# Optimization experiments

Measured on AMD Instinct MI355X. Metric: run time of the kernel, lower is better.

The kernel has to match this reference:

```python
import jax, jax.numpy as jnp
import numpy as np

T = 4096
MOL = 2048
DESC = 6
NSOL = 5
H = 2048
D_BLOCK = MOL + DESC            # 2054
FUSE = D_BLOCK * (1 + NSOL)     # 12324
D_IN = FUSE + 1                 # 12325
BOUNDARY_RF = 0.5
CLAMP_LO, CLAMP_HI = 1e-4, 1.0 - 1e-4


def setup_inputs() -> dict:
    key = jax.random.key(0)
    ks = jax.random.split(key, 32)
    s = 0.02  # weight init scale for numerical stability
    d = {
        "mol_vec": jax.random.normal(ks[0], (MOL,), jnp.float32),
        "solvent_seq": jax.random.uniform(ks[1], (T, NSOL), jnp.float32),
        "desc_seq": jax.random.normal(ks[2], (T, DESC), jnp.float32),
        "rf_true": jax.random.uniform(ks[3], (T,), jnp.float32),
        "solvent_vecs": jax.random.normal(ks[4], (NSOL, MOL), jnp.float32),
    }
    wshapes = [
        ("Wf0", (H, D_IN)), ("Wf1", (H, H)), ("Wf2", (H, H)), ("Wof", (1, H)),
        ("Wb0", (H, D_IN)), ("Wb1", (H, H)), ("Wb2", (H, H)), ("Wob", (1, H)),
    ]
    for i, (name, shp) in enumerate(wshapes):
        d[name] = jax.random.normal(ks[5 + i], shp, jnp.float32) * s
    for name, shp in [("bf0", (H,)), ("bf1", (H,)), ("bf2", (H,)), ("bof", (1,)),
                      ("bb0", (H,)), ("bb1", (H,)), ("bb2", (H,)), ("bob", (1,))]:
        d[name] = jnp.zeros(shp, jnp.float32)
    return d


def _step_features(mol_vec, solvent_seq, desc_seq, solvent_vecs):
    # mol_vec [MOL]; solvent_seq [T,NSOL]; desc_seq [T,DESC]; solvent_vecs [NSOL,MOL]
    mol_cat = jnp.concatenate(
        [jnp.broadcast_to(mol_vec, (T, MOL)), desc_seq], axis=-1)  # [T, D_BLOCK]
    scaled = solvent_seq[:, :, None] * solvent_vecs[None, :, :]      # [T,NSOL,MOL]
    sol_block = jnp.concatenate(
        [scaled, jnp.broadcast_to(desc_seq[:, None, :], (T, NSOL, DESC))], axis=-1)
    sol_flat = sol_block.reshape(T, NSOL * D_BLOCK)
    return jnp.concatenate([mol_cat, sol_flat], axis=-1)             # [T, FUSE]


def _trunk(x, W0, b0, W1, b1, W2, b2):
    # 3 Linear+GELU blocks (dropout is identity in eval)
    h = jax.nn.gelu(x @ W0.T + b0, approximate=False)
    h = jax.nn.gelu(h @ W1.T + b1, approximate=False)
    h = jax.nn.gelu(h @ W2.T + b2, approximate=False)
    return h


def reference(mol_vec, solvent_seq, desc_seq, rf_true, solvent_vecs,
              Wf0, bf0, Wf1, bf1, Wf2, bf2, Wof, bof,
              Wb0, bb0, Wb1, bb1, Wb2, bb2, Wob, bob):
    x = _step_features(mol_vec, solvent_seq, desc_seq, solvent_vecs)  # [T, FUSE]
    rf = jax.lax.stop_gradient(rf_true)  # teacher signal is detached
    b = jnp.asarray([BOUNDARY_RF], dtype=x.dtype)
    prev = jnp.concatenate([b, rf[:-1]])  # fwd branch sees rf_true[t-1]
    nxt = jnp.concatenate([rf[1:], b])    # bwd branch sees rf_true[t+1]

    inp_f = jnp.concatenate([x, prev[:, None]], axis=-1)  # [T, D_IN]
    inp_b = jnp.concatenate([x, nxt[:, None]], axis=-1)

    hf = _trunk(inp_f, Wf0, bf0, Wf1, bf1, Wf2, bf2)
    hb = _trunk(inp_b, Wb0, bb0, Wb1, bb1, Wb2, bb2)
    rf_fwd = (hf @ Wof.T + bof).squeeze(-1)  # [T]
    rf_bwd = (hb @ Wob.T + bob).squeeze(-1)
    rf_fwd = jnp.clip(rf_fwd, CLAMP_LO, CLAMP_HI)
    rf_bwd = jnp.clip(rf_bwd, CLAMP_LO, CLAMP_HI)
    return rf_fwd, rf_bwd
```

## Files before the change

kernel.cpp:

```cpp
#include <hip/hip_runtime.h>
#include <hip/hip_fp16.h>
#include <math.h>

#define T_DIM 4096
#define MOL_N 2048
#define DESC_N 6
#define NSOL_N 5
#define H_DIM 2048
#define DBLK 2054
#define D_IN_N 12325
#define GK 2048

typedef _Float16 f16x8 __attribute__((ext_vector_type(8)));
typedef float f32x4 __attribute__((ext_vector_type(4)));

__device__ __forceinline__ float gelu_f(float x) {
    float v = x * (1.5957691f + 0.0713548f * x * x);
    float e = __expf(-v);
    return x / (1.0f + e);
}

__global__ __launch_bounds__(256) void fold2_kernel(
    const float* __restrict__ W0f, const float* __restrict__ W0b,
    const float* __restrict__ b0f, const float* __restrict__ b0b,
    const float* __restrict__ mol, const float* __restrict__ sv,
    float* __restrict__ fold_f, float* __restrict__ fold_b)
{
    __shared__ float wrow[13312];
    __shared__ float red[4][6];
    const int tid = threadIdx.x;
    const int wave = tid >> 6, lane = tid & 63;
    const size_t matbytes = (size_t)2048 * D_IN_N * 4;
    char* wrc = (char*)wrow;

    for (int rr = 0; rr < 4; ++rr) {
        const int r = blockIdx.x + rr * 1024;
        const int z = r >> 11, h = r & 2047;
        const float* __restrict__ W0 = z ? W0b : W0f;
        const float* __restrict__ b0 = z ? b0b : b0f;
        float* __restrict__ fold = z ? fold_b : fold_f;
        const size_t rowdw = (size_t)h * D_IN_N;
        const size_t A0 = rowdw & ~(size_t)3;
        const int p = (int)(rowdw & 3);
        const size_t A0byte = A0 * 4;
        const char* __restrict__ W0c = (const char*)W0;

        #pragma unroll
        for (int j = 0; j < 13; ++j) {
            const size_t off = (size_t)j * 4096 + (size_t)wave * 1024 + (size_t)lane * 16;
            size_t g = A0byte + off;
            if (g + 16 > matbytes) g = A0byte;
            __builtin_amdgcn_global_load_lds(
                (const __attribute__((address_space(1))) void*)(W0c + g),
                (__attribute__((address_space(3))) void*)(wrc + off), 16, 0, 0);
        }
        asm volatile("s_waitcnt vmcnt(0)" ::: "memory");
        __syncthreads();

        float acc[6] = {0.f, 0.f, 0.f, 0.f, 0.f, 0.f};
        #pragma unroll
        for (int s = 0; s < 6; ++s) {
            const int cb = (s == 0) ? 0 : DBLK * s;
            const float* __restrict__ xp = (s == 0) ? mol : (sv + (size_t)(s - 1) * MOL_N);
            #pragma unroll
            for (int q = 0; q < 8; ++q) {
                const int col = tid + q * 256;
                acc[s] += wrow[p + cb + col] * xp[col];
            }
        }
        #pragma unroll
        for (int i = 0; i < 6; ++i) {
            float v = acc[i];
            #pragma unroll
            for (int off = 32; off >= 1; off >>= 1)
                v += __shfl_xor(v, off, 64);
            acc[i] = v;
        }
        if (lane == 0) {
            #pragma unroll
            for (int i = 0; i < 6; ++i) red[wave][i] = acc[i];
        }
        __syncthreads();
        if (tid < 6) {
            float s = red[0][tid] + red[1][tid] + red[2][tid] + red[3][tid];
            if (tid == 0) fold[h] = s + b0[h];
            else fold[(size_t)tid * H_DIM + h] = s;
        }
        if (tid >= 64 && tid < 70) {
            const int j = tid - 64;
            float w = wrow[p + MOL_N + j];
            #pragma unroll
            for (int s = 1; s <= 5; ++s) w += wrow[p + DBLK * s + MOL_N + j];
            fold[(size_t)(6 + j) * H_DIM + h] = w;
        }
        if (tid == 70) fold[(size_t)12 * H_DIM + h] = wrow[p + D_IN_N - 1];
        __syncthreads();
    }
}

__global__ __launch_bounds__(256) void conv_kernel(
    const float* __restrict__ W1f, const float* __restrict__ W2f,
    const float* __restrict__ W1b, const float* __restrict__ W2b,
    _Float16* __restrict__ Wc)
{
    const int b = blockIdx.x;
    const int z = b >> 10;
    const float* __restrict__ src = (z == 0) ? W1f : (z == 1) ? W2f : (z == 2) ? W1b : W2b;
    _Float16* __restrict__ dst = Wc + (size_t)z * H_DIM * H_DIM;
    const int base4 = (b & 1023) * 1024;
    struct h4 { _Float16 a, b, c, d; };
    #pragma unroll
    for (int k = 0; k < 4; ++k) {
        const int i4 = base4 + k * 256 + threadIdx.x;
        float4 v = ((const float4*)src)[i4];
        h4 o;
        o.a = (_Float16)v.x; o.b = (_Float16)v.y; o.c = (_Float16)v.z; o.d = (_Float16)v.w;
        ((h4*)dst)[i4] = o;
    }
}

__global__ __launch_bounds__(256) void h0_kernel(
    const float* __restrict__ fold_f, const float* __restrict__ fold_b,
    const float* __restrict__ desc, const float* __restrict__ sol,
    const float* __restrict__ rf,
    _Float16* __restrict__ h0f, _Float16* __restrict__ h0b)
{
    const int z = blockIdx.z;
    const float* __restrict__ fold = z ? fold_b : fold_f;
    _Float16* __restrict__ h0 = z ? h0b : h0f;
    const int hb = blockIdx.x * 1024 + threadIdx.x * 4;
    const int tbase = blockIdx.y * 64;

    float c0a[4], wpa[4], ua[NSOL_N][4], wda[DESC_N][4];
    {
        float4 v = *(const float4*)&fold[hb];
        c0a[0] = v.x; c0a[1] = v.y; c0a[2] = v.z; c0a[3] = v.w;
        v = *(const float4*)&fold[(size_t)12 * H_DIM + hb];
        wpa[0] = v.x; wpa[1] = v.y; wpa[2] = v.z; wpa[3] = v.w;
        #pragma unroll
        for (int s = 0; s < NSOL_N; ++s) {
            v = *(const float4*)&fold[(size_t)(1 + s) * H_DIM + hb];
            ua[s][0] = v.x; ua[s][1] = v.y; ua[s][2] = v.z; ua[s][3] = v.w;
        }
        #pragma unroll
        for (int j = 0; j < DESC_N; ++j) {
            v = *(const float4*)&fold[(size_t)(6 + j) * H_DIM + hb];
            wda[j][0] = v.x; wda[j][1] = v.y; wda[j][2] = v.z; wda[j][3] = v.w;
        }
    }

    struct h4s { _Float16 a, b, c, d; };
    for (int i = 0; i < 64; ++i) {
        const int t = tbase + i;
        float pv;
        if (z == 0) pv = (t == 0) ? 0.5f : rf[t - 1];
        else        pv = (t == T_DIM - 1) ? 0.5f : rf[t + 1];
        float sl[NSOL_N], dc[DESC_N];
        #pragma unroll
        for (int s = 0; s < NSOL_N; ++s) sl[s] = sol[t * NSOL_N + s];
        #pragma unroll
        for (int j = 0; j < DESC_N; ++j) dc[j] = desc[t * DESC_N + j];
        float o[4];
        #pragma unroll
        for (int e = 0; e < 4; ++e) {
            float pre = c0a[e] + wpa[e] * pv;
            #pragma unroll
            for (int s = 0; s < NSOL_N; ++s) pre += ua[s][e] * sl[s];
            #pragma unroll
            for (int j = 0; j < DESC_N; ++j) pre += wda[j][e] * dc[j];
            o[e] = gelu_f(pre);
        }
        h4s ov;
        ov.a = (_Float16)o[0]; ov.b = (_Float16)o[1];
        ov.c = (_Float16)o[2]; ov.d = (_Float16)o[3];
        *(h4s*)&h0[(size_t)t * H_DIM + hb] = ov;
    }
}

__device__ __forceinline__ void gemm_core256(
    const _Float16* __restrict__ A, const _Float16* __restrict__ W,
    const int m0, const int n0, char* sc, f32x4 (&acc)[8][4])
{
    const int tid = threadIdx.x;
    const int wave = tid >> 6;
    const int lane = tid & 63;
    const int t15 = lane & 15;
    const int quad = lane >> 4;
    const int wr = wave >> 2;
    const int wc = wave & 3;
    const int poff = (quad ^ ((t15 >> 1) & 3)) * 16;
    const int aoff0 = (wr * 128 + t15) * 64 + poff;
    const int boff0 = 16384 + (wc * 64 + t15) * 64 + poff;

    const _Float16* gsrc[4];
    #pragma unroll
    for (int ld = 0; ld < 4; ++ld) {
        const int j = (ld & 1) * 512 + tid;
        const int r = j >> 2;
        const int c = (j & 3) ^ ((r >> 1) & 3);
        gsrc[ld] = ((ld < 2) ? (A + (size_t)(m0 + r) * GK)
                             : (W + (size_t)(n0 + r) * GK)) + c * 8;
    }

    #pragma unroll
    for (int mi = 0; mi < 8; ++mi)
        #pragma unroll
        for (int ni = 0; ni < 4; ++ni)
            acc[mi][ni] = (f32x4){0.f, 0.f, 0.f, 0.f};

#define STAGE_T(kt, b) do { \
    char* _db = sc + (b) * 32768; \
    const int _ko = (kt) * 32; \
    __builtin_amdgcn_global_load_lds((const __attribute__((address_space(1))) void*)(gsrc[0] + _ko), (__attribute__((address_space(3))) void*)(_db + wave * 1024), 16, 0, 0); \
    __builtin_amdgcn_global_load_lds((const __attribute__((address_space(1))) void*)(gsrc[1] + _ko), (__attribute__((address_space(3))) void*)(_db + 8192 + wave * 1024), 16, 0, 0); \
    __builtin_amdgcn_global_load_lds((const __attribute__((address_space(1))) void*)(gsrc[2] + _ko), (__attribute__((address_space(3))) void*)(_db + 16384 + wave * 1024), 16, 0, 0); \
    __builtin_amdgcn_global_load_lds((const __attribute__((address_space(1))) void*)(gsrc[3] + _ko), (__attribute__((address_space(3))) void*)(_db + 24576 + wave * 1024), 16, 0, 0); \
} while (0)

#define COMPUTE_T(b) do { \
    const char* _db = sc + (b) * 32768; \
    f16x8 aF[8], bF[4]; \
    _Pragma("unroll") \
    for (int mi = 0; mi < 8; ++mi) aF[mi] = *(const f16x8*)(_db + aoff0 + mi * 1024); \
    _Pragma("unroll") \
    for (int ni = 0; ni < 4; ++ni) bF[ni] = *(const f16x8*)(_db + boff0 + ni * 1024); \
    __builtin_amdgcn_s_setprio(1); \
    _Pragma("unroll") \
    for (int mi = 0; mi < 8; ++mi) { \
        _Pragma("unroll") \
        for (int ni = 0; ni < 4; ++ni) \
            acc[mi][ni] = __builtin_amdgcn_mfma_f32_16x16x32_f16(aF[mi], bF[ni], acc[mi][ni], 0, 0, 0); \
    } \
    __builtin_amdgcn_s_setprio(0); \
    asm volatile("s_waitcnt lgkmcnt(0)" ::: "memory"); \
} while (0)

    STAGE_T(0, 0); STAGE_T(1, 1); STAGE_T(2, 2);

    #pragma unroll 1
    for (int k4 = 0; k4 < 60; k4 += 4) {
        asm volatile("s_waitcnt vmcnt(8)" ::: "memory");
        __builtin_amdgcn_s_barrier();
        STAGE_T(k4 + 3, 3); COMPUTE_T(0);
        asm volatile("s_waitcnt vmcnt(8)" ::: "memory");
        __builtin_amdgcn_s_barrier();
        STAGE_T(k4 + 4, 0); COMPUTE_T(1);
        asm volatile("s_waitcnt vmcnt(8)" ::: "memory");
        __builtin_amdgcn_s_barrier();
        STAGE_T(k4 + 5, 1); COMPUTE_T(2);
        asm volatile("s_waitcnt vmcnt(8)" ::: "memory");
        __builtin_amdgcn_s_barrier();
        STAGE_T(k4 + 6, 2); COMPUTE_T(3);
    }
    asm volatile("s_waitcnt vmcnt(8)" ::: "memory");
    __builtin_amdgcn_s_barrier();
    STAGE_T(63, 3); COMPUTE_T(0);
    asm volatile("s_waitcnt vmcnt(8)" ::: "memory");
    __builtin_amdgcn_s_barrier();
    COMPUTE_T(1);
    asm volatile("s_waitcnt vmcnt(4)" ::: "memory");
    __builtin_amdgcn_s_barrier();
    COMPUTE_T(2);
    asm volatile("s_waitcnt vmcnt(0)" ::: "memory");
    __builtin_amdgcn_s_barrier();
    COMPUTE_T(3);

#undef STAGE_T
#undef COMPUTE_T
}

__global__ __launch_bounds__(512, 2) void gemm1_kernel(
    const _Float16* __restrict__ Af, const _Float16* __restrict__ Ab,
    const _Float16* __restrict__ Wfp, const _Float16* __restrict__ Wbp,
    const float* __restrict__ bfp, const float* __restrict__ bbp,
    _Float16* __restrict__ Cf, _Float16* __restrict__ Cb)
{
    __shared__ _Float16 smem[65536];
    char* sc = (char*)smem;
    const int bid = blockIdx.x;
    const int xcd = bid & 7;
    const int slot = bid >> 3;
    const int z = xcd & 1;
    const int q = xcd >> 1;
    const int m0 = (q * 4 + (slot & 3)) * 256;
    const int n0 = (slot >> 2) * 256;

    const _Float16* __restrict__ A = z ? Ab : Af;
    const _Float16* __restrict__ W = z ? Wbp : Wfp;
    const float* __restrict__ bias = z ? bbp : bfp;
    _Float16* __restrict__ C = z ? Cb : Cf;

    f32x4 acc[8][4];
    gemm_core256(A, W, m0, n0, sc, acc);

    const int tid = threadIdx.x;
    const int wave = tid >> 6, lane = tid & 63;
    const int colC = lane & 15, quad = lane >> 4;
    const int wr = wave >> 2, wc = wave & 3;
    #pragma unroll
    for (int ni = 0; ni < 4; ++ni) {
        const int n = n0 + wc * 64 + ni * 16 + colC;
        const float bv = bias[n];
        #pragma unroll
        for (int mi = 0; mi < 8; ++mi) {
            const int mb = m0 + wr * 128 + mi * 16 + quad * 4;
            #pragma unroll
            for (int r = 0; r < 4; ++r)
                C[(size_t)(mb + r) * H_DIM + n] = (_Float16)gelu_f(acc[mi][ni][r] + bv);
        }
    }
}

__global__ __launch_bounds__(512, 2) void gemm_out_kernel(
    const _Float16* __restrict__ Af, const _Float16* __restrict__ Ab,
    const _Float16* __restrict__ Wfp, const _Float16* __restrict__ Wbp,
    const float* __restrict__ bfp, const float* __restrict__ bbp,
    const float* __restrict__ Wof, const float* __restrict__ Wob,
    float* __restrict__ partial)
{
    __shared__ _Float16 smem[65536];
    char* sc = (char*)smem;
    const int bid = blockIdx.x;
    const int xcd = bid & 7;
    const int slot = bid >> 3;
    const int z = xcd & 1;
    const int q = xcd >> 1;
    const int m0 = (q * 4 + (slot & 3)) * 256;
    const int n0 = (slot >> 2) * 256;

    const _Float16* __restrict__ A = z ? Ab : Af;
    const _Float16* __restrict__ W = z ? Wbp : Wfp;
    const float* __restrict__ bias = z ? bbp : bfp;
    const float* __restrict__ Wo = z ? Wob : Wof;

    f32x4 acc[8][4];
    gemm_core256(A, W, m0, n0, sc, acc);

    const int tid = threadIdx.x;
    const int wave = tid >> 6, lane = tid & 63;
    const int colC = lane & 15, quad = lane >> 4;
    const int wr = wave >> 2, wc = wave & 3;

    float bv[4], wo[4];
    #pragma unroll
    for (int ni = 0; ni < 4; ++ni) {
        const int n = n0 + wc * 64 + ni * 16 + colC;
        bv[ni] = bias[n];
        wo[ni] = Wo[n];
    }

    __syncthreads();
    float* red = (float*)sc;
    #pragma unroll
    for (int mi = 0; mi < 8; ++mi) {
        #pragma unroll
        for (int r = 0; r < 4; ++r) {
            float s = 0.f;
            #pragma unroll
            for (int ni = 0; ni < 4; ++ni)
                s += gelu_f(acc[mi][ni][r] + bv[ni]) * wo[ni];
            s += __shfl_xor(s, 1, 64);
            s += __shfl_xor(s, 2, 64);
            s += __shfl_xor(s, 4, 64);
            s += __shfl_xor(s, 8, 64);
            if (colC == 0)
                red[wc * 256 + wr * 128 + mi * 16 + quad * 4 + r] = s;
        }
    }
    __syncthreads();
    if (tid < 256) {
        float v = red[tid] + red[256 + tid] + red[512 + tid] + red[768 + tid];
        const int n_tile = slot >> 2;
        partial[((size_t)z * 8 + n_tile) * T_DIM + m0 + tid] = v;
    }
}

__global__ __launch_bounds__(256) void finalize_kernel(
    const float* __restrict__ partial,
    const float* __restrict__ bof, const float* __restrict__ bob,
    float* __restrict__ out)
{
    const int idx = blockIdx.x * 256 + threadIdx.x;
    const int z = idx >> 12;
    const int row = idx & 4095;
    float v = z ? bob[0] : bof[0];
    #pragma unroll
    for (int nt = 0; nt < 8; ++nt)
        v += partial[((size_t)z * 8 + nt) * T_DIM + row];
    v = fminf(fmaxf(v, 1e-4f), 1.0f - 1e-4f);
    out[idx] = v;
}

extern "C" void kernel_launch(void* const* d_in, const int* in_sizes, int n_in,
                              void* d_out, int out_size, void* d_ws, size_t ws_size,
                              hipStream_t stream)
{
    (void)in_sizes; (void)n_in; (void)out_size; (void)ws_size;
    const float* mol = (const float*)d_in[0];
    const float* sol = (const float*)d_in[1];
    const float* desc = (const float*)d_in[2];
    const float* rf  = (const float*)d_in[3];
    const float* sv  = (const float*)d_in[4];
    const float* Wf0 = (const float*)d_in[5];
    const float* Wf1 = (const float*)d_in[6];
    const float* Wf2 = (const float*)d_in[7];
    const float* Wof = (const float*)d_in[8];
    const float* Wb0 = (const float*)d_in[9];
    const float* Wb1 = (const float*)d_in[10];
    const float* Wb2 = (const float*)d_in[11];
    const float* Wob = (const float*)d_in[12];
    const float* bf0 = (const float*)d_in[13];
    const float* bf1 = (const float*)d_in[14];
    const float* bf2 = (const float*)d_in[15];
    const float* bof = (const float*)d_in[16];
    const float* bb0 = (const float*)d_in[17];
    const float* bb1 = (const float*)d_in[18];
    const float* bb2 = (const float*)d_in[19];
    const float* bob = (const float*)d_in[20];
    float* out = (float*)d_out;

    char* ws = (char*)d_ws;
    float* fold_f = (float*)(ws + 0);
    float* fold_b = (float*)(ws + 131072);
    _Float16* Wc = (_Float16*)(ws + 262144);
    const size_t WSZ = (size_t)H_DIM * H_DIM;
    _Float16* W1f_c = Wc;
    _Float16* W2f_c = Wc + WSZ;
    _Float16* W1b_c = Wc + 2 * WSZ;
    _Float16* W2b_c = Wc + 3 * WSZ;
    const size_t HSZ = (size_t)T_DIM * H_DIM;
    _Float16* h0f = (_Float16*)(ws + 33816576);
    _Float16* h0b = h0f + HSZ;
    _Float16* h1f = (_Float16*)(ws + 33816576 + 2 * 16777216);
    _Float16* h1b = h1f + HSZ;
    float* partial = (float*)(ws + 33816576);

    fold2_kernel<<<dim3(1024), 256, 0, stream>>>(Wf0, Wb0, bf0, bb0, mol, sv, fold_f, fold_b);
    conv_kernel<<<dim3(4096), 256, 0, stream>>>(Wf1, Wf2, Wb1, Wb2, Wc);
    h0_kernel<<<dim3(2, 64, 2), 256, 0, stream>>>(fold_f, fold_b, desc, sol, rf, h0f, h0b);
    gemm1_kernel<<<dim3(256), 512, 0, stream>>>(h0f, h0b, W1f_c, W1b_c, bf1, bb1, h1f, h1b);
    gemm_out_kernel<<<dim3(256), 512, 0, stream>>>(h1f, h1b, W2f_c, W2b_c, bf2, bb2, Wof, Wob, partial);
    finalize_kernel<<<dim3(32), 256, 0, stream>>>(partial, bof, bob, out);
}
```

Before: 469.8 us.

## Split fold kernel across row-segments grid and remap GEMM tiles per XCD

The first-layer weight fold kernel, which looped over 4 rows per block with an LDS staging buffer, is replaced by a 4096x6 grid where each block reduces one 2048-column segment of one row straight from global memory. This raises parallelism and removes the 52KB LDS footprint, which should help the bandwidth-bound read of the two large first-layer weight matrices, at the cost of more blocks and unaligned global reads. The GEMM block-to-tile mapping also changes so that each XCD covers all M tiles for two N tiles rather than four M tiles for all N tiles, which changes L2 reuse of the weight versus activation panels.

Result: slower. 487.3 us (+3.7%).

```diff
diff --git a/kernel.cpp b/kernel.cpp
--- a/kernel.cpp
+++ b/kernel.cpp
@@ -20,81 +20,51 @@
     return x / (1.0f + e);
 }
 
-__global__ __launch_bounds__(256) void fold2_kernel(
+__global__ __launch_bounds__(256) void fold3_kernel(
     const float* __restrict__ W0f, const float* __restrict__ W0b,
     const float* __restrict__ b0f, const float* __restrict__ b0b,
     const float* __restrict__ mol, const float* __restrict__ sv,
     float* __restrict__ fold_f, float* __restrict__ fold_b)
 {
-    __shared__ float wrow[13312];
-    __shared__ float red[4][6];
+    __shared__ float red[4];
+    const int r = blockIdx.x;
+    const int s = blockIdx.y;
+    const int z = r >> 11, h = r & 2047;
     const int tid = threadIdx.x;
-    const int wave = tid >> 6, lane = tid & 63;
-    const size_t matbytes = (size_t)2048 * D_IN_N * 4;
-    char* wrc = (char*)wrow;
-
-    for (int rr = 0; rr < 4; ++rr) {
-        const int r = blockIdx.x + rr * 1024;
-        const int z = r >> 11, h = r & 2047;
-        const float* __restrict__ W0 = z ? W0b : W0f;
-        const float* __restrict__ b0 = z ? b0b : b0f;
-        float* __restrict__ fold = z ? fold_b : fold_f;
-        const size_t rowdw = (size_t)h * D_IN_N;
-        const size_t A0 = rowdw & ~(size_t)3;
-        const int p = (int)(rowdw & 3);
-        const size_t A0byte = A0 * 4;
-        const char* __restrict__ W0c = (const char*)W0;
-
-        #pragma unroll
-        for (int j = 0; j < 13; ++j) {
-            const size_t off = (size_t)j * 4096 + (size_t)wave * 1024 + (size_t)lane * 16;
-            size_t g = A0byte + off;
-            if (g + 16 > matbytes) g = A0byte;
-            __builtin_amdgcn_global_load_lds(
-                (const __attribute__((address_space(1))) void*)(W0c + g),
-                (__attribute__((address_space(3))) void*)(wrc + off), 16, 0, 0);
-        }
-        asm volatile("s_waitcnt vmcnt(0)" ::: "memory");
-        __syncthreads();
-
-        float acc[6] = {0.f, 0.f, 0.f, 0.f, 0.f, 0.f};
-        #pragma unroll
-        for (int s = 0; s < 6; ++s) {
-            const int cb = (s == 0) ? 0 : DBLK * s;
-            const float* __restrict__ xp = (s == 0) ? mol : (sv + (size_t)(s - 1) * MOL_N);
-            #pragma unroll
-            for (int q = 0; q < 8; ++q) {
-                const int col = tid + q * 256;
-                acc[s] += wrow[p + cb + col] * xp[col];
-            }
-        }
-        #pragma unroll
-        for (int i = 0; i < 6; ++i) {
-            float v = acc[i];
-            #pragma unroll
-            for (int off = 32; off >= 1; off >>= 1)
-                v += __shfl_xor(v, off, 64);
-            acc[i] = v;
-        }
-        if (lane == 0) {
-            #pragma unroll
-            for (int i = 0; i < 6; ++i) red[wave][i] = acc[i];
-        }
-        __syncthreads();
-        if (tid < 6) {
-            float s = red[0][tid] + red[1][tid] + red[2][tid] + red[3][tid];
-            if (tid == 0) fold[h] = s + b0[h];
-            else fold[(size_t)tid * H_DIM + h] = s;
-        }
-        if (tid >= 64 && tid < 70) {
-            const int j = tid - 64;
-            float w = wrow[p + MOL_N + j];
-            #pragma unroll
-            for (int s = 1; s <= 5; ++s) w += wrow[p + DBLK * s + MOL_N + j];
-            fold[(size_t)(6 + j) * H_DIM + h] = w;
-        }
-        if (tid == 70) fold[(size_t)12 * H_DIM + h] = wrow[p + D_IN_N - 1];
-        __syncthreads();
+    const float* __restrict__ W0 = z ? W0b : W0f;
+    const float* __restrict__ b0 = z ? b0b : b0f;
+    float* __restrict__ fold = z ? fold_b : fold_f;
+    const float* __restrict__ row = W0 + (size_t)h * D_IN_N + (size_t)s * DBLK;
+    const float* __restrict__ xp = (s == 0) ? mol : (sv + (size_t)(s - 1) * MOL_N);
+
+    float acc = 0.f;
+    #pragma unroll
+    for (int k = 0; k < 8; ++k) {
+        const int c = tid + k * 256;
+        acc += row[c] * xp[c];
+    }
+    #pragma unroll
+    for (int off = 32; off >= 1; off >>= 1)
+        acc += __shfl_xor(acc, off, 64);
+    const int lane = tid & 63, wave = tid >> 6;
+    if (lane == 0) red[wave] = acc;
+    __syncthreads();
+    if (tid == 0) {
+        float v = red[0] + red[1] + red[2] + red[3];
+        if (s == 0) fold[h] = v + b0[h];
+        else fold[(size_t)s * H_DIM + h] = v;
+    }
+    if (s == 0 && tid >= 64 && tid < 70) {
+        const int j = tid - 64;
+        const float* __restrict__ rw = W0 + (size_t)h * D_IN_N;
+        float w = rw[MOL_N + j];
+        #pragma unroll
+        for (int ss = 1; ss <= 5; ++ss) w += rw[(size_t)DBLK * ss + MOL_N + j];
+        fold[(size_t)(6 + j) * H_DIM + h] = w;
+    }
+    if (s == 0 && tid == 70) {
+        const float* __restrict__ rw = W0 + (size_t)h * D_IN_N;
+        fold[(size_t)12 * H_DIM + h] = rw[D_IN_N - 1];
     }
 }
 
@@ -269,6 +239,17 @@
 #undef COMPUTE_T
 }
 
+__device__ __forceinline__ void tile_map(int bid, int& z, int& m0, int& n0, int& n_tile)
+{
+    const int xcd = bid & 7;
+    const int slot = bid >> 3;
+    z = xcd & 1;
+    const int q = xcd >> 1;
+    m0 = (slot & 15) * 256;
+    n_tile = q * 2 + (slot >> 4);
+    n0 = n_tile * 256;
+}
+
 __global__ __launch_bounds__(512, 2) void gemm1_kernel(
     const _Float16* __restrict__ Af, const _Float16* __restrict__ Ab,
     const _Float16* __restrict__ Wfp, const _Float16* __restrict__ Wbp,
@@ -277,13 +258,8 @@
 {
     __shared__ _Float16 smem[65536];
     char* sc = (char*)smem;
-    const int bid = blockIdx.x;
-    const int xcd = bid & 7;
-    const int slot = bid >> 3;
-    const int z = xcd & 1;
-    const int q = xcd >> 1;
-    const int m0 = (q * 4 + (slot & 3)) * 256;
-    const int n0 = (slot >> 2) * 256;
+    int z, m0, n0, n_tile;
+    tile_map(blockIdx.x, z, m0, n0, n_tile);
 
     const _Float16* __restrict__ A = z ? Ab : Af;
     const _Float16* __restrict__ W = z ? Wbp : Wfp;
@@ -320,13 +296,8 @@
 {
     __shared__ _Float16 smem[65536];
     char* sc = (char*)smem;
-    const int bid = blockIdx.x;
-    const int xcd = bid & 7;
-    const int slot = bid >> 3;
-    const int z = xcd & 1;
-    const int q = xcd >> 1;
-    const int m0 = (q * 4 + (slot & 3)) * 256;
-    const int n0 = (slot >> 2) * 256;
+    int z, m0, n0, n_tile;
+    tile_map(blockIdx.x, z, m0, n0, n_tile);
 
     const _Float16* __restrict__ A = z ? Ab : Af;
     const _Float16* __restrict__ W = z ? Wbp : Wfp;
@@ -370,7 +341,6 @@
     __syncthreads();
     if (tid < 256) {
         float v = red[tid] + red[256 + tid] + red[512 + tid] + red[768 + tid];
-        const int n_tile = slot >> 2;
         partial[((size_t)z * 8 + n_tile) * T_DIM + m0 + tid] = v;
     }
 }
@@ -435,7 +405,7 @@
     _Float16* h1b = h1f + HSZ;
     float* partial = (float*)(ws + 33816576);
 
-    fold2_kernel<<<dim3(1024), 256, 0, stream>>>(Wf0, Wb0, bf0, bb0, mol, sv, fold_f, fold_b);
+    fold3_kernel<<<dim3(4096, 6), 256, 0, stream>>>(Wf0, Wb0, bf0, bb0, mol, sv, fold_f, fold_b);
     conv_kernel<<<dim3(4096), 256, 0, stream>>>(Wf1, Wf2, Wb1, Wb2, Wc);
     h0_kernel<<<dim3(2, 64, 2), 256, 0, stream>>>(fold_f, fold_b, desc, sol, rf, h0f, h0b);
     gemm1_kernel<<<dim3(256), 512, 0, stream>>>(h0f, h0b, W1f_c, W1b_c, bf1, bb1, h1f, h1b);
```
